# Kernel tuning notes

Measured on AMD Instinct MI355X. Metric: run time of the kernel, lower is better.

## Reference

```python
import jax, jax.numpy as jnp
import numpy as np

B, S, D = 1, 2048, 2048
H, KVH, HD = 16, 8, 128
ROPE_THETA = 1e6
P_POW, C_SHIFT = 8, 7.0
MASK_VAL = -7.0  # = -c so masked bpmax base ~ scores only (finite under ^8)


def rotate_half(x):
    x1, x2 = jnp.split(x, 2, axis=-1)
    return jnp.concatenate([-x2, x1], axis=-1)


def setup_inputs() -> dict:
    key = jax.random.key(0)
    ks = jax.random.split(key, 10)
    hidden_states = jax.random.normal(ks[0], (B, S, D), dtype=jnp.float32)
    # RoPE tables (Qwen3-style, theta=1e6)
    inv_freq = 1.0 / (ROPE_THETA ** (jnp.arange(0, HD, 2, dtype=jnp.float32) / HD))
    freqs = jnp.arange(S, dtype=jnp.float32)[:, None] * inv_freq[None, :]
    emb = jnp.concatenate([freqs, freqs], axis=-1)  # [S, HD]
    cos = jnp.broadcast_to(jnp.cos(emb)[None], (B, S, HD)).astype(jnp.float32)
    sin = jnp.broadcast_to(jnp.sin(emb)[None], (B, S, HD)).astype(jnp.float32)
    sc = D ** -0.5
    q_proj_w = jax.random.normal(ks[1], (D, H * HD), dtype=jnp.float32) * sc
    k_proj_w = jax.random.normal(ks[2], (D, KVH * HD), dtype=jnp.float32) * sc
    v_proj_w = jax.random.normal(ks[3], (D, KVH * HD), dtype=jnp.float32) * sc
    o_proj_w = jax.random.normal(ks[4], (H * HD, D), dtype=jnp.float32) * (H * HD) ** -0.5
    q_norm_w = jnp.ones((HD,), dtype=jnp.float32)
    k_norm_w = jnp.ones((HD,), dtype=jnp.float32)
    # Stored RMSNorm denominators (rsqrt-like buffers from training), ~O(1)
    q_denom = 0.5 + jax.random.uniform(ks[5], (B, S, H, 1), dtype=jnp.float32)
    k_denom = 0.5 + jax.random.uniform(ks[6], (B, S, KVH, 1), dtype=jnp.float32)
    # Stored bpmax normalizer buffer rd (per-head, per-query-row)
    rd = 5.0 + 10.0 * jax.random.uniform(ks[7], (1, H, S, 1), dtype=jnp.float32)
    # Causal mask with MASK_VAL for masked positions (finite under bpmax)
    causal = jnp.tril(jnp.ones((S, S), dtype=bool))
    attention_mask = jnp.where(causal, 0.0, MASK_VAL)[None, None].astype(jnp.float32)
    return {
        'hidden_states': hidden_states, 'cos': cos, 'sin': sin,
        'q_proj_w': q_proj_w, 'k_proj_w': k_proj_w, 'v_proj_w': v_proj_w,
        'o_proj_w': o_proj_w, 'q_norm_w': q_norm_w, 'k_norm_w': k_norm_w,
        'q_denom': q_denom, 'k_denom': k_denom, 'rd': rd,
        'attention_mask': attention_mask,
    }


def reference(hidden_states, cos, sin, q_proj_w, k_proj_w, v_proj_w, o_proj_w,
              q_norm_w, k_norm_w, q_denom, k_denom, rd, attention_mask):
    b, s, d = hidden_states.shape
    hd = q_norm_w.shape[0]
    scaling = hd ** -0.5
    # Projections + per-head RMSNorm (eval path: stored denominator buffer)
    q = (hidden_states @ q_proj_w).reshape(b, s, -1, hd)
    q = (q_norm_w * (q * q_denom[:, :s])).transpose(0, 2, 1, 3)   # [B,H,S,hd]
    k = (hidden_states @ k_proj_w).reshape(b, s, -1, hd)
    k = (k_norm_w * (k * k_denom[:, :s])).transpose(0, 2, 1, 3)   # [B,KVH,S,hd]
    v = (hidden_states @ v_proj_w).reshape(b, s, -1, hd).transpose(0, 2, 1, 3)
    # RoPE
    cos_ = cos[:, None, :, :]
    sin_ = sin[:, None, :, :]
    q = q * cos_ + rotate_half(q) * sin_
    k = k * cos_ + rotate_half(k) * sin_
    # GQA: repeat kv heads
    groups = q.shape[1] // k.shape[1]
    k = jnp.repeat(k, groups, axis=1)
    v = jnp.repeat(v, groups, axis=1)
    # Scores + mask + bpmax power-law normalization (eval path)
    aw = jnp.einsum('bhqd,bhkd->bhqk', q, k) * scaling
    aw = aw + attention_mask[:, :, :, :s]
    aw = ((aw + C_SHIFT) / rd[:, :, :s, :]) ** P_POW
    # Attention output + output projection
    out = jnp.einsum('bhqk,bhkd->bhqd', aw, v)
    out = out.transpose(0, 2, 1, 3).reshape(b, s, -1)
    return out @ o_proj_w
```

## Files before the change

kernel.cpp:

```cpp
#include <hip/hip_runtime.h>
#include <cstdint>
#include <cstddef>


namespace {
constexpr int kS = 2048;
constexpr int kD = 2048;
constexpr int kH = 16;
constexpr int kKVH = 8;
constexpr int kHD = 128;
constexpr float kScale = 0.08838834764831845f;
constexpr size_t MB = 1u << 20;
}

using f32x4 = __attribute__((ext_vector_type(4))) float;
using bfrag = __attribute__((ext_vector_type(8))) short;
using float4v = __attribute__((ext_vector_type(4))) float;
using short4v = __attribute__((ext_vector_type(4))) short;

__device__ __forceinline__ unsigned short f2b(float f) {
  union { float f; unsigned u; } x; x.f = f;
  unsigned r = x.u + 0x7FFFu + ((x.u >> 16) & 1u);
  return (unsigned short)(r >> 16);
}

__device__ __forceinline__ void gload_lds16(const void* g, void* l) {
  __builtin_amdgcn_global_load_lds(
      (const __attribute__((address_space(1))) unsigned*)g,
      (__attribute__((address_space(3))) unsigned*)l, 16, 0, 0);
}

__global__ __launch_bounds__(256) void qwen_cast_bf16(const float* __restrict__ in,
                                                      unsigned short* __restrict__ out,
                                                      int n4) {
  int i = blockIdx.x * 256 + threadIdx.x;
  if (i >= n4) return;
  float4v v = *(const float4v*)(in + (size_t)i * 4);
  short4v o;
  o[0] = (short)f2b(v[0]); o[1] = (short)f2b(v[1]);
  o[2] = (short)f2b(v[2]); o[3] = (short)f2b(v[3]);
  *(short4v*)(out + (size_t)i * 4) = o;
}

__global__ __launch_bounds__(256) void qwen_tw(const float* __restrict__ in, int R, int C,
                                               unsigned short* __restrict__ out, int ldo) {
  __shared__ float t[64][65];
  int c0 = blockIdx.x * 64, r0 = blockIdx.y * 64;
  int tr = threadIdx.x >> 6, tc = threadIdx.x & 63;
#pragma unroll
  for (int p = 0; p < 16; ++p) {
    int i = p * 4 + tr;
    t[i][tc] = in[(size_t)(r0 + i) * C + c0 + tc];
  }
  __syncthreads();
#pragma unroll
  for (int p = 0; p < 16; ++p) {
    int i = p * 4 + tr;
    out[(size_t)(c0 + i) * ldo + r0 + tc] = f2b(t[tc][i]);
  }
}

template <int BM>
__global__ __launch_bounds__(256) void qwen_gemm_bt(const unsigned short* __restrict__ A,
                                                    const unsigned short* __restrict__ Bt,
                                                    float* __restrict__ C,
                                                    int M, int N, int K) {
  __shared__ unsigned short As[BM * 32];
  __shared__ unsigned short Bs[128 * 32];
  constexpr int MR = BM / 32;
  const int nwg = gridDim.x * gridDim.y;
  int lin = blockIdx.y * gridDim.x + blockIdx.x;
  if ((nwg & 7) == 0) { int qq = nwg >> 3; lin = (lin & 7) * qq + (lin >> 3); }
  const int bxx = lin % gridDim.x, byy = lin / gridDim.x;
  const int tid = threadIdx.x, lane = tid & 63, w = tid >> 6;
  const int wr = w >> 1, wc = w & 1;
  const int row0 = bxx * BM, col0 = byy * 128;
  f32x4 acc[MR][4] = {};
  const int koff = (lane >> 4) << 3;
  const int rA = wr * (BM / 2) + (lane & 15);
  const int rB = wc * 64 + (lane & 15);
  for (int kt = 0; kt < K; kt += 32) {
#pragma unroll
    for (int c = 0; c < BM / 64; ++c) {
      int off = (c * 256 + tid) * 16;
      int e = off >> 1;
      int r = e >> 5, cc = e & 31;
      gload_lds16(A + (size_t)(row0 + r) * K + kt + cc, (char*)As + off);
    }
#pragma unroll
    for (int c = 0; c < 2; ++c) {
      int off = (c * 256 + tid) * 16;
      int e = off >> 1;
      int r = e >> 5, cc = e & 31;
      gload_lds16(Bt + (size_t)(col0 + r) * K + kt + cc, (char*)Bs + off);
    }
    __syncthreads();
    bfrag aF[MR], bF[4];
#pragma unroll
    for (int m = 0; m < MR; ++m) aF[m] = *(const bfrag*)(As + (rA + m * 16) * 32 + koff);
#pragma unroll
    for (int n = 0; n < 4; ++n) bF[n] = *(const bfrag*)(Bs + (rB + n * 16) * 32 + koff);
#pragma unroll
    for (int m = 0; m < MR; ++m)
#pragma unroll
      for (int n = 0; n < 4; ++n)
        acc[m][n] = __builtin_amdgcn_mfma_f32_16x16x32_bf16(aF[m], bF[n], acc[m][n], 0, 0, 0);
    __syncthreads();
  }
  const int cr = (lane >> 4) << 2;
  const int cc2 = lane & 15;
#pragma unroll
  for (int m = 0; m < MR; ++m)
#pragma unroll
    for (int n = 0; n < 4; ++n) {
      int r = row0 + wr * (BM / 2) + m * 16 + cr;
      int c = col0 + wc * 64 + n * 16 + cc2;
#pragma unroll
      for (int j = 0; j < 4; ++j) C[(size_t)(r + j) * N + c] = acc[m][n][j];
    }
}

__global__ __launch_bounds__(256) void qwen_rope_qk(const float* __restrict__ Cqkv,
                                                    const float* __restrict__ cosb,
                                                    const float* __restrict__ sinb,
                                                    const float* __restrict__ qnw,
                                                    const float* __restrict__ knw,
                                                    const float* __restrict__ qden,
                                                    const float* __restrict__ kden,
                                                    unsigned short* __restrict__ Qb,
                                                    unsigned short* __restrict__ Kswz) {
  int s = blockIdx.x;
  int t = threadIdx.x;
  const float* row = Cqkv + (size_t)s * 4096;
  const float* cs = cosb + (size_t)s * kHD;
  const float* sn = sinb + (size_t)s * kHD;
#pragma unroll
  for (int rep = 0; rep < 8; ++rep) {
    int idx = rep * 256 + t;
    int h = idx >> 7, d = idx & 127;
    float dn = qden[s * kH + h];
    float v = row[idx] * dn * qnw[d];
    float pv = row[(h << 7) + (d ^ 64)] * dn * qnw[d ^ 64];
    float rot = (d < 64) ? -pv : pv;
    Qb[((size_t)h * kS + s) * kHD + d] = f2b(v * cs[d] + rot * sn[d]);
  }
  const int kt = s >> 6, key = s & 63;
#pragma unroll
  for (int rep = 0; rep < 4; ++rep) {
    int idx = rep * 256 + t;
    int h = idx >> 7, d = idx & 127;
    float dn = kden[s * kKVH + h];
    float v = row[2048 + idx] * dn * knw[d];
    float pv = row[2048 + (h << 7) + (d ^ 64)] * dn * knw[d ^ 64];
    float rot = (d < 64) ? -pv : pv;
    size_t rowi = ((size_t)(h * 32 + kt) * 64 + key) * 128;
    Kswz[rowi + (d ^ ((key & 7) << 3))] = f2b(v * cs[d] + rot * sn[d]);
  }
}

__global__ __launch_bounds__(256) void qwen_vtr(const float* __restrict__ Cqkv,
                                                unsigned short* __restrict__ Vswz) {
  __shared__ float t[64][65];
  int kvh = blockIdx.x, st = blockIdx.y, dt = blockIdx.z;
  int s0 = st * 64, d0 = dt * 64;
  int tr = threadIdx.x >> 6, tc = threadIdx.x & 63;
#pragma unroll
  for (int p = 0; p < 16; ++p) {
    int i = p * 4 + tr;
    t[i][tc] = Cqkv[(size_t)(s0 + i) * 4096 + 3072 + (kvh << 7) + d0 + tc];
  }
  __syncthreads();
#pragma unroll
  for (int p = 0; p < 16; ++p) {
    int i = p * 4 + tr;
    int d = d0 + i;
    size_t rowi = ((size_t)(kvh * 32 + st) * 128 + d) * 64;
    Vswz[rowi + (tc ^ ((d & 7) << 2))] = f2b(t[tc][i]);
  }
}

#define STAGE8(cc, bb)                                                 \
  do {                                                                 \
    const char* ks_ = Ksrc + ((size_t)(cc) << 14) + tid * 16;          \
    const char* vs_ = Vsrc + ((size_t)(cc) << 14) + tid * 16;          \
    char* kd_ = (char*)(&KV[bb][0]) + tid * 16;                        \
    char* vd_ = (char*)(&KV[2 + (bb)][0]) + tid * 16;                  \
    _Pragma("unroll") for (int it = 0; it < 4; ++it) {                 \
      gload_lds16(ks_ + it * 4096, kd_ + it * 4096);                   \
      gload_lds16(vs_ + it * 4096, vd_ + it * 4096);                   \
    }                                                                  \
  } while (0)

__global__ __launch_bounds__(256, 2) void qwen_attn(const unsigned short* __restrict__ Qb,
                                                    const unsigned short* __restrict__ Kswz,
                                                    const unsigned short* __restrict__ Vswz,
                                                    const float* __restrict__ rd,
                                                    unsigned short* __restrict__ AO) {
  __shared__ unsigned short KV[4][8192];
  const int bid = blockIdx.x;
  const int kvh = bid & 7;
  const int h = kvh * 2 + ((bid >> 3) & 1);
  const int qt = 31 - (bid >> 4);
  const int q0 = qt * 64;
  const int nch = qt + 1;
  const int tid = threadIdx.x, lane = tid & 63, w = tid >> 6;
  const int l15 = lane & 15, g = lane >> 4;
  const int qw0 = q0 + w * 16;
  const int qlim = qw0 + l15;
  const int swzK = (l15 & 7) << 3;
  const int swzV = (l15 & 7) << 2;

  bfrag qF[4];
#pragma unroll
  for (int dc = 0; dc < 4; ++dc)
    qF[dc] = *(const bfrag*)(Qb + ((size_t)h * kS + qw0 + l15) * kHD + dc * 32 + g * 8);
  const float inv = 1.0f / rd[(size_t)h * kS + qw0 + l15];

  const char* Ksrc = (const char*)Kswz + ((size_t)(kvh * 32) << 14);
  const char* Vsrc = (const char*)Vswz + ((size_t)(kvh * 32) << 14);

  f32x4 outa[8] = {};

  STAGE8(0, 0);
#pragma unroll 1
  for (int c = 0; c < nch; ++c) {
    const int b = c & 1;
    if (c + 1 < nch) {
      STAGE8(c + 1, b ^ 1);
      asm volatile("s_waitcnt vmcnt(8)" ::: "memory");
    } else {
      asm volatile("s_waitcnt vmcnt(0)" ::: "memory");
    }
    __builtin_amdgcn_s_barrier();
    const unsigned short* Kbuf = &KV[b][0];
    const unsigned short* Vbuf = &KV[2 + b][0];
    f32x4 sc[4] = {};
#pragma unroll
    for (int t = 0; t < 4; ++t) {
      const unsigned short* kr = Kbuf + (t * 16 + l15) * 128;
#pragma unroll
      for (int dc = 0; dc < 4; ++dc) {
        bfrag kf = *(const bfrag*)(kr + ((dc * 32 + g * 8) ^ swzK));
        sc[t] = __builtin_amdgcn_mfma_f32_16x16x32_bf16(kf, qF[dc], sc[t], 0, 0, 0);
      }
    }
    const int kbase = c * 64;
    const bool full = (c < qt);
    union { bfrag f; unsigned u[4]; } pb[2];
#pragma unroll
    for (int t = 0; t < 4; ++t) {
      unsigned short bb[4];
#pragma unroll
      for (int rr = 0; rr < 4; ++rr) {
        float tt = sc[t][rr] * kScale;
        int key = kbase + t * 16 + g * 4 + rr;
        tt += (full || key <= qlim) ? 7.0f : 0.0f;
        float y = tt * inv;
        float y2 = y * y, y4 = y2 * y2;
        bb[rr] = f2b(y4 * y4);
      }
      pb[t >> 1].u[(t & 1) * 2 + 0] = (unsigned)bb[0] | ((unsigned)bb[1] << 16);
      pb[t >> 1].u[(t & 1) * 2 + 1] = (unsigned)bb[2] | ((unsigned)bb[3] << 16);
    }
#pragma unroll
    for (int dt = 0; dt < 8; ++dt) {
      const unsigned short* vr = Vbuf + (dt * 16 + l15) * 64;
#pragma unroll
      for (int pr = 0; pr < 2; ++pr) {
        union { bfrag f; short4v h4[2]; } va;
        va.h4[0] = *(const short4v*)(vr + ((pr * 32 + g * 4) ^ swzV));
        va.h4[1] = *(const short4v*)(vr + ((pr * 32 + 16 + g * 4) ^ swzV));
        outa[dt] = __builtin_amdgcn_mfma_f32_16x16x32_bf16(va.f, pb[pr].f, outa[dt], 0, 0, 0);
      }
    }
    __builtin_amdgcn_s_barrier();
  }
#pragma unroll
  for (int dt = 0; dt < 8; ++dt) {
    short4v o;
    o[0] = (short)f2b(outa[dt][0]); o[1] = (short)f2b(outa[dt][1]);
    o[2] = (short)f2b(outa[dt][2]); o[3] = (short)f2b(outa[dt][3]);
    *(short4v*)(AO + (size_t)(qw0 + l15) * kD + h * 128 + dt * 16 + g * 4) = o;
  }
}

extern "C" void kernel_launch(void* const* d_in, const int* in_sizes, int n_in,
                              void* d_out, int out_size, void* d_ws, size_t ws_size,
                              hipStream_t stream) {
  (void)in_sizes; (void)n_in; (void)out_size; (void)ws_size;
  const float* hidden = (const float*)d_in[0];
  const float* cosb   = (const float*)d_in[1];
  const float* sinb   = (const float*)d_in[2];
  const float* qw     = (const float*)d_in[3];
  const float* kw     = (const float*)d_in[4];
  const float* vw     = (const float*)d_in[5];
  const float* ow     = (const float*)d_in[6];
  const float* qnw    = (const float*)d_in[7];
  const float* knw    = (const float*)d_in[8];
  const float* qden   = (const float*)d_in[9];
  const float* kden   = (const float*)d_in[10];
  const float* rd     = (const float*)d_in[11];
  float* out = (float*)d_out;

  char* ws = (char*)d_ws;
  unsigned short* hsb  = (unsigned short*)(ws + 0 * MB);
  unsigned short* Wt   = (unsigned short*)(ws + 8 * MB);
  float*          Cqkv = (float*)(ws + 24 * MB);
  unsigned short* Qb   = (unsigned short*)(ws + 56 * MB);
  unsigned short* Kswz = (unsigned short*)(ws + 64 * MB);
  unsigned short* Vswz = (unsigned short*)(ws + 68 * MB);
  unsigned short* AO   = (unsigned short*)(ws + 72 * MB);
  unsigned short* Ot   = (unsigned short*)(ws + 80 * MB);

  qwen_cast_bf16<<<4096, 256, 0, stream>>>(hidden, hsb, 2048 * 2048 / 4);
  qwen_tw<<<dim3(32, 32), 256, 0, stream>>>(qw, 2048, 2048, Wt, 2048);
  qwen_tw<<<dim3(16, 32), 256, 0, stream>>>(kw, 2048, 1024, Wt + (size_t)2048 * 2048, 2048);
  qwen_tw<<<dim3(16, 32), 256, 0, stream>>>(vw, 2048, 1024, Wt + (size_t)3072 * 2048, 2048);
  qwen_tw<<<dim3(32, 32), 256, 0, stream>>>(ow, 2048, 2048, Ot, 2048);
  qwen_gemm_bt<128><<<dim3(16, 32), 256, 0, stream>>>(hsb, Wt, Cqkv, 2048, 4096, 2048);
  qwen_rope_qk<<<2048, 256, 0, stream>>>(Cqkv, cosb, sinb, qnw, knw, qden, kden, Qb, Kswz);
  qwen_vtr<<<dim3(8, 32, 2), 256, 0, stream>>>(Cqkv, Vswz);
  qwen_attn<<<512, 256, 0, stream>>>(Qb, Kswz, Vswz, rd, AO);
  qwen_gemm_bt<64><<<dim3(32, 16), 256, 0, stream>>>(AO, Ot, out, 2048, 2048, 2048);
}
```

Baseline: 184.5 us.

## Double-buffer GEMM LDS tiles and use larger tile for output projection

The bf16 GEMM kernel now keeps two LDS buffers and issues the global-to-LDS loads for the next K-slice before running the MFMAs on the current one, with a single vmcnt wait and barrier per iteration. This is meant to overlap memory latency with matrix math instead of waiting for loads then computing. The output projection also moves from 64-row to 128-row tiles, halving the workgroup count to 256. That raises per-block reuse but lowers occupancy and parallelism on a GPU with many CUs, and LDS use per block doubles.

Result: faster. 180.7 us (-2.1%).

```diff
diff --git a/kernel.cpp b/kernel.cpp
--- a/kernel.cpp
+++ b/kernel.cpp
@@ -65,8 +65,8 @@
                                                     const unsigned short* __restrict__ Bt,
                                                     float* __restrict__ C,
                                                     int M, int N, int K) {
-  __shared__ unsigned short As[BM * 32];
-  __shared__ unsigned short Bs[128 * 32];
+  __shared__ unsigned short As[2][BM * 32];
+  __shared__ unsigned short Bs[2][128 * 32];
   constexpr int MR = BM / 32;
   const int nwg = gridDim.x * gridDim.y;
   int lin = blockIdx.y * gridDim.x + blockIdx.x;
@@ -79,33 +79,47 @@
   const int koff = (lane >> 4) << 3;
   const int rA = wr * (BM / 2) + (lane & 15);
   const int rB = wc * 64 + (lane & 15);
-  for (int kt = 0; kt < K; kt += 32) {
+
+  auto stage = [&](int kt, int b) {
 #pragma unroll
     for (int c = 0; c < BM / 64; ++c) {
       int off = (c * 256 + tid) * 16;
       int e = off >> 1;
       int r = e >> 5, cc = e & 31;
-      gload_lds16(A + (size_t)(row0 + r) * K + kt + cc, (char*)As + off);
+      gload_lds16(A + (size_t)(row0 + r) * K + kt + cc, (char*)(&As[b][0]) + off);
     }
 #pragma unroll
     for (int c = 0; c < 2; ++c) {
       int off = (c * 256 + tid) * 16;
       int e = off >> 1;
       int r = e >> 5, cc = e & 31;
-      gload_lds16(Bt + (size_t)(col0 + r) * K + kt + cc, (char*)Bs + off);
-    }
-    __syncthreads();
+      gload_lds16(Bt + (size_t)(col0 + r) * K + kt + cc, (char*)(&Bs[b][0]) + off);
+    }
+  };
+
+  const int nk = K >> 5;
+  stage(0, 0);
+  asm volatile("s_waitcnt vmcnt(0)" ::: "memory");
+  __builtin_amdgcn_s_barrier();
+  int buf = 0;
+#pragma unroll 1
+  for (int t = 0; t < nk; ++t) {
+    if (t + 1 < nk) stage((t + 1) << 5, buf ^ 1);
     bfrag aF[MR], bF[4];
 #pragma unroll
-    for (int m = 0; m < MR; ++m) aF[m] = *(const bfrag*)(As + (rA + m * 16) * 32 + koff);
-#pragma unroll
-    for (int n = 0; n < 4; ++n) bF[n] = *(const bfrag*)(Bs + (rB + n * 16) * 32 + koff);
+    for (int m = 0; m < MR; ++m)
+      aF[m] = *(const bfrag*)(&As[buf][0] + (rA + m * 16) * 32 + koff);
+#pragma unroll
+    for (int n = 0; n < 4; ++n)
+      bF[n] = *(const bfrag*)(&Bs[buf][0] + (rB + n * 16) * 32 + koff);
 #pragma unroll
     for (int m = 0; m < MR; ++m)
 #pragma unroll
       for (int n = 0; n < 4; ++n)
         acc[m][n] = __builtin_amdgcn_mfma_f32_16x16x32_bf16(aF[m], bF[n], acc[m][n], 0, 0, 0);
-    __syncthreads();
+    asm volatile("s_waitcnt vmcnt(0)" ::: "memory");
+    __builtin_amdgcn_s_barrier();
+    buf ^= 1;
   }
   const int cr = (lane >> 4) << 2;
   const int cc2 = lane & 15;
@@ -321,5 +335,5 @@
   qwen_rope_qk<<<2048, 256, 0, stream>>>(Cqkv, cosb, sinb, qnw, knw, qden, kden, Qb, Kswz);
   qwen_vtr<<<dim3(8, 32, 2), 256, 0, stream>>>(Cqkv, Vswz);
   qwen_attn<<<512, 256, 0, stream>>>(Qb, Kswz, Vswz, rd, AO);
-  qwen_gemm_bt<64><<<dim3(32, 16), 256, 0, stream>>>(AO, Ot, out, 2048, 2048, 2048);
-}
+  qwen_gemm_bt<128><<<dim3(16, 16), 256, 0, stream>>>(AO, Ot, out, 2048, 2048, 2048);
+}
```
